# Optimization experiments

Hardware: AMD Instinct MI355X
Metric: run time of the kernel (lower is better)

## Reference

```python
import jax, jax.numpy as jnp
import numpy as np

B, P, T = 128, 196, 20
VOCAB, ENC, EMB, DEC, ATTN = 10000, 2048, 512, 512, 512


def _linear_params(key, out_dim, in_dim):
    kw, kb = jax.random.split(key)
    s = 1.0 / np.sqrt(in_dim)
    W = jax.random.uniform(kw, (out_dim, in_dim), minval=-s, maxval=s, dtype=jnp.float32)
    b = jax.random.uniform(kb, (out_dim,), minval=-s, maxval=s, dtype=jnp.float32)
    return W, b


def setup_inputs() -> dict:
    key = jax.random.key(0)
    ks = jax.random.split(key, 12)
    enc_w, enc_b = _linear_params(ks[0], ATTN, ENC)
    dec_w, dec_b = _linear_params(ks[1], ATTN, DEC)
    full_w, full_b = _linear_params(ks[2], 1, ATTN)
    W_ih, b_ih = _linear_params(ks[3], 4 * DEC, EMB + ENC)
    W_hh, b_hh = _linear_params(ks[4], 4 * DEC, DEC)
    ih_w, ih_b = _linear_params(ks[5], DEC, ENC)
    ic_w, ic_b = _linear_params(ks[6], DEC, ENC)
    fc_w, fc_b = _linear_params(ks[7], VOCAB, DEC)
    return {
        "encoder_out": jax.random.normal(ks[8], (B, P, ENC), dtype=jnp.float32),
        "captions": jax.random.randint(ks[9], (B, T), 0, VOCAB, dtype=jnp.int32),
        "lengths": jax.random.randint(ks[10], (B,), 1, T + 1, dtype=jnp.int32),
        "embedding": jax.random.normal(ks[11], (VOCAB, EMB), dtype=jnp.float32),
        "enc_attn_w": enc_w, "enc_attn_b": enc_b,
        "dec_attn_w": dec_w, "dec_attn_b": dec_b,
        "full_attn_w": full_w, "full_attn_b": full_b,
        "W_ih": W_ih, "b_ih": b_ih, "W_hh": W_hh, "b_hh": b_hh,
        "init_h_w": ih_w, "init_h_b": ih_b,
        "init_c_w": ic_w, "init_c_b": ic_b,
        "fc_w": fc_w, "fc_b": fc_b,
    }


def reference(encoder_out, captions, lengths, embedding,
              enc_attn_w, enc_attn_b, dec_attn_w, dec_attn_b,
              full_attn_w, full_attn_b, W_ih, b_ih, W_hh, b_hh,
              init_h_w, init_h_b, init_c_w, init_c_b, fc_w, fc_b):
    # init hidden state from mean-pooled encoder features
    mean_enc = encoder_out.mean(axis=1)                      # [B, ENC]
    h = mean_enc @ init_h_w.T + init_h_b                      # [B, DEC]
    c = mean_enc @ init_c_w.T + init_c_b

    # loop-invariant encoder projection for additive attention
    attn_enc = jnp.einsum('bpe,ae->bpa', encoder_out, enc_attn_w) + enc_attn_b  # [B, P, ATTN]

    embs = embedding[captions]                                # [B, T, EMB]
    embs_t = jnp.swapaxes(embs, 0, 1)                         # [T, B, EMB]

    dec = h.shape[1]

    def step(carry, emb_t):
        h, c = carry
        # additive attention
        attn_dec = h @ dec_attn_w.T + dec_attn_b              # [B, ATTN]
        energy = jnp.einsum('bpa,a->bp', jax.nn.relu(attn_enc + attn_dec[:, None, :]), full_attn_w[0]) + full_attn_b[0]
        alpha = jax.nn.softmax(energy, axis=1)                # [B, P]
        context = jnp.einsum('bpe,bp->be', encoder_out, alpha)  # [B, ENC]
        # LSTMCell
        x = jnp.concatenate([emb_t, context], axis=1)
        gates = x @ W_ih.T + b_ih + h @ W_hh.T + b_hh          # [B, 4*DEC]
        i, f, g, o = jnp.split(gates, 4, axis=1)
        c_new = jax.nn.sigmoid(f) * c + jax.nn.sigmoid(i) * jnp.tanh(g)
        h_new = jax.nn.sigmoid(o) * jnp.tanh(c_new)
        preds = h_new @ fc_w.T + fc_b                          # [B, VOCAB] (dropout in eval mode = identity)
        return (h_new, c_new), (preds, alpha)

    (_, _), (outputs_t, alphas_t) = jax.lax.scan(step, (h, c), embs_t)
    outputs = jnp.swapaxes(outputs_t, 0, 1)                   # [B, T, VOCAB]
    alphas = jnp.swapaxes(alphas_t, 0, 1)                     # [B, T, P]
    return outputs, alphas
```

## Files before the change

kernel.cpp:

```cpp
#include <hip/hip_runtime.h>

constexpr int kB = 128, kP = 196, kT = 20;
constexpr int kVocab = 10000, kEnc = 2048, kEmb = 512, kDec = 512, kAttn = 512;

typedef __bf16 b16x8 __attribute__((ext_vector_type(8)));
typedef __bf16 b16x4 __attribute__((ext_vector_type(4)));
typedef float f32x4 __attribute__((ext_vector_type(4)));
typedef unsigned short u16x4 __attribute__((ext_vector_type(4)));

__device__ __forceinline__ unsigned short f2bf(float f) {
  unsigned int u = __float_as_uint(f);
  u += 0x7fffu + ((u >> 16) & 1u);
  return (unsigned short)(u >> 16);
}
__device__ __forceinline__ float bf2f(unsigned short h) {
  return __uint_as_float(((unsigned int)h) << 16);
}

__device__ __forceinline__ void async16(const void* g, void* l) {
  __builtin_amdgcn_global_load_lds(
      (const __attribute__((address_space(1))) unsigned int*)g,
      (__attribute__((address_space(3))) unsigned int*)l, 16, 0, 0);
}

template <int MODE>
__global__ __launch_bounds__(256) void gemm128(
    const unsigned short* __restrict__ A, const unsigned short* __restrict__ W,
    const float* __restrict__ bias, unsigned short* __restrict__ Cb,
    float* __restrict__ Cf, int K, int Nv) {
  __shared__ unsigned short sA[128 * 32];
  __shared__ unsigned short sB[128 * 32];
  const int tid = threadIdx.x;
  const int lane = tid & 63, wave = tid >> 6;
  const int wm = wave >> 1, wn = wave & 1;
  const int q = lane >> 4, l = lane & 15;
  const int m0 = blockIdx.y * 128, n0 = blockIdx.x * 128;
  const int row0 = tid & 127, ch0 = tid >> 7;
  const long arow = (long)(m0 + row0) * K + ch0 * 8;
  const long brow = (long)(n0 + row0) * K + ch0 * 8;
  unsigned short* sAd0 = &sA[(ch0 * 128 + row0) * 8];
  unsigned short* sAd1 = &sA[((ch0 + 2) * 128 + row0) * 8];
  unsigned short* sBd0 = &sB[(ch0 * 128 + row0) * 8];
  unsigned short* sBd1 = &sB[((ch0 + 2) * 128 + row0) * 8];
  f32x4 acc[4][4] = {};

  for (int k0 = 0; k0 < K; k0 += 32) {
    async16(A + arow + k0, sAd0);
    async16(A + arow + k0 + 16, sAd1);
    async16(W + brow + k0, sBd0);
    async16(W + brow + k0 + 16, sBd1);
    __syncthreads();
    b16x8 af[4], bf[4];
#pragma unroll
    for (int i = 0; i < 4; i++)
      af[i] = *(const b16x8*)&sA[(q * 128 + wm * 64 + 16 * i + l) * 8];
#pragma unroll
    for (int j = 0; j < 4; j++)
      bf[j] = *(const b16x8*)&sB[(q * 128 + wn * 64 + 16 * j + l) * 8];
#pragma unroll
    for (int i = 0; i < 4; i++)
#pragma unroll
      for (int j = 0; j < 4; j++)
        acc[i][j] = __builtin_amdgcn_mfma_f32_16x16x32_bf16(af[i], bf[j], acc[i][j], 0, 0, 0);
    __syncthreads();
  }

#pragma unroll
  for (int i = 0; i < 4; i++) {
    const int row = m0 + wm * 64 + 16 * i + q * 4;
#pragma unroll
    for (int j = 0; j < 4; j++) {
      const int col = n0 + wn * 64 + 16 * j + l;
      if (col >= Nv) continue;
      const float bv = bias[col];
#pragma unroll
      for (int r = 0; r < 4; r++) {
        const float v = acc[i][j][r] + bv;
        if (MODE == 0) {
          Cb[(long)(row + r) * kAttn + col] = f2bf(v);
        } else {
          const int rr = row + r;
          Cf[((long)(rr & 127) * kT + (rr >> 7)) * (long)kVocab + col] = v;
        }
      }
    }
  }
}

template <bool A_BF16, bool OUT_BF16>
__global__ __launch_bounds__(256) void gemm_bt(
    const void* __restrict__ A_, const unsigned short* __restrict__ W,
    const float* __restrict__ bias, float* __restrict__ C,
    unsigned short* __restrict__ Cb, int M, int N, int K, long ldc) {
  const int lane = threadIdx.x & 63;
  const int wave = threadIdx.x >> 6;
  const int wm = wave >> 1, wn = wave & 1;
  const int m0 = blockIdx.y * 64 + wm * 32;
  const int n0 = blockIdx.x * 64 + wn * 32;
  const int q = lane >> 4;
  const int l = lane & 15;
  f32x4 acc[2][2] = {};
  const unsigned short* Ab = (const unsigned short*)A_;
  const float* Af = (const float*)A_;

  for (int k0 = 0; k0 < K; k0 += 32) {
    const int ka = k0 + q * 8;
    b16x8 af[2], wf[2];
#pragma unroll
    for (int i = 0; i < 2; i++) {
      int r = m0 + 16 * i + l;
      if (r >= M) r = M - 1;
      if (A_BF16) {
        af[i] = *(const b16x8*)(Ab + (long)r * K + ka);
      } else {
        const float* p = Af + (long)r * K + ka;
        const f32x4 lo = *(const f32x4*)p;
        const f32x4 hi = *(const f32x4*)(p + 4);
        b16x8 t;
#pragma unroll
        for (int j = 0; j < 4; j++) {
          ((unsigned short*)&t)[j] = f2bf(lo[j]);
          ((unsigned short*)&t)[4 + j] = f2bf(hi[j]);
        }
        af[i] = t;
      }
    }
#pragma unroll
    for (int j = 0; j < 2; j++) {
      int r = n0 + 16 * j + l;
      if (r >= N) r = N - 1;
      wf[j] = *(const b16x8*)(W + (long)r * K + ka);
    }
#pragma unroll
    for (int i = 0; i < 2; i++)
#pragma unroll
      for (int j = 0; j < 2; j++)
        acc[i][j] = __builtin_amdgcn_mfma_f32_16x16x32_bf16(af[i], wf[j], acc[i][j], 0, 0, 0);
  }

#pragma unroll
  for (int i = 0; i < 2; i++)
#pragma unroll
    for (int j = 0; j < 2; j++) {
      const int col = n0 + 16 * j + l;
      if (col >= N) continue;
      const float bv = bias ? bias[col] : 0.0f;
#pragma unroll
      for (int r = 0; r < 4; r++) {
        const int row = m0 + 16 * i + q * 4 + r;
        if (row >= M) continue;
        const float v = acc[i][j][r] + bv;
        if (OUT_BF16) Cb[(long)row * ldc + col] = f2bf(v);
        else          C[(long)row * ldc + col] = v;
      }
    }
}

__global__ __launch_bounds__(256) void adfc_kernel(
    const unsigned short* __restrict__ h_bf,
    const unsigned short* __restrict__ daw, const float* __restrict__ dab,
    float* __restrict__ ad_out,
    const unsigned short* __restrict__ fcw, const float* __restrict__ fcb,
    float* __restrict__ preds, long pred_ld) {
  const int blk = blockIdx.x;
  const unsigned short* W;
  const float* bias;
  float* out;
  long ldc;
  int N, m0, n0;
  if (blk < 16) {
    if (!ad_out) return;
    W = daw; bias = dab; out = ad_out; ldc = 512; N = 512;
    n0 = (blk & 7) * 64; m0 = (blk >> 3) * 64;
  } else {
    if (!preds) return;
    const int idx = blk - 16;
    W = fcw; bias = fcb; out = preds; ldc = pred_ld; N = kVocab;
    n0 = (idx % 157) * 64; m0 = (idx / 157) * 64;
  }
  const int lane = threadIdx.x & 63, wave = threadIdx.x >> 6;
  const int wm = wave >> 1, wn = wave & 1;
  const int q = lane >> 4, l = lane & 15;
  const int mi = m0 + wm * 32, ni = n0 + wn * 32;
  f32x4 acc[2][2] = {};

  for (int k0 = 0; k0 < 512; k0 += 64) {
    b16x8 af[2][2], wf[2][2];
#pragma unroll
    for (int u = 0; u < 2; u++) {
      const int ka = k0 + u * 32 + q * 8;
#pragma unroll
      for (int i = 0; i < 2; i++)
        af[u][i] = *(const b16x8*)(h_bf + (long)(mi + 16 * i + l) * 512 + ka);
#pragma unroll
      for (int j = 0; j < 2; j++) {
        int r = ni + 16 * j + l;
        if (r >= N) r = N - 1;
        wf[u][j] = *(const b16x8*)(W + (long)r * 512 + ka);
      }
    }
#pragma unroll
    for (int u = 0; u < 2; u++)
#pragma unroll
      for (int i = 0; i < 2; i++)
#pragma unroll
        for (int j = 0; j < 2; j++)
          acc[i][j] = __builtin_amdgcn_mfma_f32_16x16x32_bf16(af[u][i], wf[u][j], acc[i][j], 0, 0, 0);
  }
#pragma unroll
  for (int i = 0; i < 2; i++)
#pragma unroll
    for (int j = 0; j < 2; j++) {
      const int col = ni + 16 * j + l;
      if (col >= N) continue;
      const float bv = bias[col];
#pragma unroll
      for (int r = 0; r < 4; r++) {
        const int row = mi + 16 * i + q * 4 + r;
        out[(long)row * ldc + col] = acc[i][j][r] + bv;
      }
    }
}

template <bool SRC_BF16>
__global__ __launch_bounds__(256) void attn2(
    const void* __restrict__ enc_, const unsigned short* __restrict__ attn_enc_bf,
    const float* __restrict__ ad_g, const float* __restrict__ faw,
    const float* __restrict__ fab, float* __restrict__ alphas,
    unsigned short* __restrict__ ctx, int t) {
  const int b = blockIdx.x;
  const int half = blockIdx.y;
  const int tid = threadIdx.x;
  const int lane = tid & 63, wave = tid >> 6;
  __shared__ float ad_s[512];
  __shared__ float e_sm[kP];
  __shared__ float red[4];
  __shared__ float cred[128][8];

  ad_s[tid] = ad_g[b * kAttn + tid];
  ad_s[tid + 256] = ad_g[b * kAttn + tid + 256];
  __syncthreads();

  float ad8[8], w8[8];
  const int a0 = lane * 8;
#pragma unroll
  for (int j = 0; j < 8; j++) { ad8[j] = ad_s[a0 + j]; w8[j] = faw[a0 + j]; }
  const float fb0 = fab[0];
  for (int p = wave; p < kP; p += 4) {
    const b16x8 rv = *(const b16x8*)(attn_enc_bf + ((long)(b * kP + p)) * kAttn + a0);
    float s = 0.f;
#pragma unroll
    for (int j = 0; j < 8; j++)
      s += w8[j] * fmaxf(bf2f(((const unsigned short*)&rv)[j]) + ad8[j], 0.f);
#pragma unroll
    for (int off = 32; off > 0; off >>= 1) s += __shfl_down(s, off, 64);
    if (lane == 0) e_sm[p] = s + fb0;
  }
  __syncthreads();

  const float v = (tid < kP) ? e_sm[tid] : -3.0e38f;
  float m = v;
#pragma unroll
  for (int off = 32; off > 0; off >>= 1) m = fmaxf(m, __shfl_down(m, off, 64));
  if (lane == 0) red[wave] = m;
  __syncthreads();
  m = fmaxf(fmaxf(red[0], red[1]), fmaxf(red[2], red[3]));
  const float ex = (tid < kP) ? expf(v - m) : 0.f;
  float s = ex;
#pragma unroll
  for (int off = 32; off > 0; off >>= 1) s += __shfl_down(s, off, 64);
  if (lane == 0) red[wave] = s;
  __syncthreads();
  s = red[0] + red[1] + red[2] + red[3];
  __syncthreads();
  const float alpha = ex / s;
  if (tid < kP) {
    e_sm[tid] = alpha;
    if (half == 0) alphas[((long)b * kT + t) * kP + tid] = alpha;
  }
  __syncthreads();

  const int pg = tid >> 7, th = tid & 127;
  const int e = half * 1024 + th * 8;
  float a8[8] = {};
  if (SRC_BF16) {
    const unsigned short* base = (const unsigned short*)enc_ + (long)b * kP * kEnc + e;
    const int pbeg = pg * 98;
#pragma unroll 2
    for (int p = pbeg; p < pbeg + 98; p++) {
      const float a = e_sm[p];
      const b16x8 rv = *(const b16x8*)(base + (long)p * kEnc);
#pragma unroll
      for (int j = 0; j < 8; j++) a8[j] += a * bf2f(((const unsigned short*)&rv)[j]);
    }
  } else {
    const float* base = (const float*)enc_ + (long)b * kP * kEnc + e;
    const int pbeg = pg * 98;
#pragma unroll 2
    for (int p = pbeg; p < pbeg + 98; p++) {
      const float a = e_sm[p];
      const f32x4 lo = *(const f32x4*)(base + (long)p * kEnc);
      const f32x4 hi = *(const f32x4*)(base + (long)p * kEnc + 4);
#pragma unroll
      for (int j = 0; j < 4; j++) { a8[j] += a * lo[j]; a8[4 + j] += a * hi[j]; }
    }
  }
  if (pg == 1) {
#pragma unroll
    for (int j = 0; j < 8; j++) cred[th][j] = a8[j];
  }
  __syncthreads();
  if (pg == 0) {
    u16x4 o0, o1;
#pragma unroll
    for (int j = 0; j < 4; j++) {
      o0[j] = f2bf(a8[j] + cred[th][j]);
      o1[j] = f2bf(a8[4 + j] + cred[th][4 + j]);
    }
    *(u16x4*)(ctx + (long)b * kEnc + e) = o0;
    *(u16x4*)(ctx + (long)b * kEnc + e + 4) = o1;
  }
}

__global__ __launch_bounds__(256) void gemm_gates(
    const unsigned short* __restrict__ embs_t, const unsigned short* __restrict__ ctx,
    const unsigned short* __restrict__ hbf, const unsigned short* __restrict__ Wih,
    const unsigned short* __restrict__ Whh, float* __restrict__ gates_part) {
  const int lane = threadIdx.x & 63;
  const int wave = threadIdx.x >> 6;
  const int wm = wave >> 1, wn = wave & 1;
  const int m0 = blockIdx.y * 64 + wm * 32;
  const int n0 = blockIdx.x * 64 + wn * 32;
  const int z = blockIdx.z;
  const int q = lane >> 4;
  const int l = lane & 15;
  f32x4 acc[2][2] = {};
  float* gout = gates_part + (long)z * kB * 2048;

  const int kbeg = z * 768, kend = kbeg + 768;
  for (int k0 = kbeg; k0 < kend; k0 += 32) {
    b16x8 af[2], wf[2];
#pragma unroll
    for (int i = 0; i < 2; i++) {
      const int r = m0 + 16 * i + l;
      const unsigned short* p;
      if (k0 < 512)        p = embs_t + (long)r * kEmb + k0;
      else if (k0 < 2560)  p = ctx + (long)r * kEnc + (k0 - 512);
      else                 p = hbf + (long)r * kDec + (k0 - 2560);
      af[i] = *(const b16x8*)(p + q * 8);
    }
#pragma unroll
    for (int j = 0; j < 2; j++) {
      const int r = n0 + 16 * j + l;
      const unsigned short* p;
      if (k0 < 2560) p = Wih + (long)r * 2560 + k0;
      else           p = Whh + (long)r * 512 + (k0 - 2560);
      wf[j] = *(const b16x8*)(p + q * 8);
    }
#pragma unroll
    for (int i = 0; i < 2; i++)
#pragma unroll
      for (int j = 0; j < 2; j++)
        acc[i][j] = __builtin_amdgcn_mfma_f32_16x16x32_bf16(af[i], wf[j], acc[i][j], 0, 0, 0);
  }
#pragma unroll
  for (int i = 0; i < 2; i++)
#pragma unroll
    for (int j = 0; j < 2; j++) {
      const int col = n0 + 16 * j + l;
#pragma unroll
      for (int r = 0; r < 4; r++) {
        const int row = m0 + 16 * i + q * 4 + r;
        gout[(long)row * 2048 + col] = acc[i][j][r];
      }
    }
}

__global__ __launch_bounds__(256) void lstm_pw(
    const float* __restrict__ gp, const float* __restrict__ bsum,
    float* __restrict__ c, float* __restrict__ h, unsigned short* __restrict__ hbf) {
  const int idx = blockIdx.x * 256 + threadIdx.x;
  const int b = idx >> 9, d = idx & 511;
  float g4[4];
#pragma unroll
  for (int g = 0; g < 4; g++) {
    const int col = g * 512 + d;
    float s = bsum[col];
#pragma unroll
    for (int z = 0; z < 4; z++) s += gp[(long)z * kB * 2048 + (long)b * 2048 + col];
    g4[g] = s;
  }
  const float si = 1.f / (1.f + expf(-g4[0]));
  const float sf = 1.f / (1.f + expf(-g4[1]));
  const float so = 1.f / (1.f + expf(-g4[3]));
  const float cn = sf * c[idx] + si * tanhf(g4[2]);
  const float hn = so * tanhf(cn);
  c[idx] = cn;
  h[idx] = hn;
  hbf[idx] = f2bf(hn);
}

template <bool SRC_BF16>
__global__ __launch_bounds__(256) void mean_kernel(
    const void* __restrict__ enc_, unsigned short* __restrict__ mean_bf) {
  const int b = blockIdx.x;
  const int e = threadIdx.x * 8;
  float acc[8] = {};
  if (SRC_BF16) {
    const unsigned short* base = (const unsigned short*)enc_ + (long)b * kP * kEnc + e;
    for (int p = 0; p < kP; p++) {
      const b16x8 v = *(const b16x8*)(base + (long)p * kEnc);
#pragma unroll
      for (int j = 0; j < 8; j++) acc[j] += bf2f(((const unsigned short*)&v)[j]);
    }
  } else {
    const float* base = (const float*)enc_ + (long)b * kP * kEnc + e;
    for (int p = 0; p < kP; p++) {
      const f32x4 lo = *(const f32x4*)(base + (long)p * kEnc);
      const f32x4 hi = *(const f32x4*)(base + (long)p * kEnc + 4);
#pragma unroll
      for (int j = 0; j < 4; j++) { acc[j] += lo[j]; acc[4 + j] += hi[j]; }
    }
  }
#pragma unroll
  for (int j = 0; j < 8; j++)
    mean_bf[(long)b * kEnc + e + j] = f2bf(acc[j] * (1.0f / 196.0f));
}

__global__ __launch_bounds__(256) void f32_to_bf16_vec(
    const float* __restrict__ src, unsigned short* __restrict__ dst, long n4) {
  for (long i = blockIdx.x * (long)blockDim.x + threadIdx.x; i < n4;
       i += (long)gridDim.x * blockDim.x) {
    const f32x4 v = *(const f32x4*)(src + i * 4);
    u16x4 o;
#pragma unroll
    for (int j = 0; j < 4; j++) o[j] = f2bf(v[j]);
    *(u16x4*)(dst + i * 4) = o;
  }
}

__global__ __launch_bounds__(256) void gather_emb(
    const float* __restrict__ embedding, const int* __restrict__ captions,
    unsigned short* __restrict__ embs) {
  const int r = blockIdx.x;
  const int t = r >> 7, b = r & 127;
  const int cap = captions[b * kT + t];
  const float* src = embedding + (long)cap * kEmb;
  unsigned short* dst = embs + (long)r * kEmb;
  for (int i = threadIdx.x; i < kEmb; i += 256) dst[i] = f2bf(src[i]);
}

__global__ void bias_sum_k(const float* __restrict__ b1, const float* __restrict__ b2,
                           float* __restrict__ o) {
  const int i = blockIdx.x * 256 + threadIdx.x;
  if (i < 2048) o[i] = b1[i] + b2[i];
}

extern "C" void kernel_launch(void* const* d_in, const int* in_sizes, int n_in,
                              void* d_out, int out_size, void* d_ws, size_t ws_size,
                              hipStream_t stream) {
  const float* enc = (const float*)d_in[0];
  const int* captions = (const int*)d_in[1];
  const float* embedding = (const float*)d_in[3];
  const float* eaw = (const float*)d_in[4];
  const float* eab = (const float*)d_in[5];
  const float* daw = (const float*)d_in[6];
  const float* dab = (const float*)d_in[7];
  const float* faw = (const float*)d_in[8];
  const float* fab = (const float*)d_in[9];
  const float* Wih = (const float*)d_in[10];
  const float* bih = (const float*)d_in[11];
  const float* Whh = (const float*)d_in[12];
  const float* bhh = (const float*)d_in[13];
  const float* ihw = (const float*)d_in[14];
  const float* ihb = (const float*)d_in[15];
  const float* icw = (const float*)d_in[16];
  const float* icb = (const float*)d_in[17];
  const float* fcw = (const float*)d_in[18];
  const float* fcb = (const float*)d_in[19];

  float* out = (float*)d_out;
  float* alphas = out + (long)kB * kT * kVocab;

  char* ws = (char*)d_ws;
  size_t off = 0;
  auto alloc = [&](size_t bytes) -> void* {
    void* p = ws + off;
    off = (off + bytes + 255) & ~(size_t)255;
    return p;
  };
  unsigned short* attn_enc_bf = (unsigned short*)alloc((size_t)kB * kP * kAttn * 2);
  unsigned short* Wih_bf = (unsigned short*)alloc((size_t)2048 * 2560 * 2);
  unsigned short* Whh_bf = (unsigned short*)alloc((size_t)2048 * 512 * 2);
  unsigned short* fcw_bf = (unsigned short*)alloc((size_t)kVocab * kDec * 2);
  unsigned short* eaw_bf = (unsigned short*)alloc((size_t)kAttn * kEnc * 2);
  unsigned short* daw_bf = (unsigned short*)alloc((size_t)kAttn * kDec * 2);
  unsigned short* ihw_bf = (unsigned short*)alloc((size_t)kDec * kEnc * 2);
  unsigned short* icw_bf = (unsigned short*)alloc((size_t)kDec * kEnc * 2);
  unsigned short* embs_bf = (unsigned short*)alloc((size_t)kT * kB * kEmb * 2);
  unsigned short* mean_bf = (unsigned short*)alloc((size_t)kB * kEnc * 2);
  float* h = (float*)alloc((size_t)kB * kDec * 4);
  float* c = (float*)alloc((size_t)kB * kDec * 4);
  unsigned short* h_hist = (unsigned short*)alloc((size_t)(kT + 1) * kB * kDec * 2);
  float* ad_buf = (float*)alloc((size_t)kB * kAttn * 4);
  unsigned short* ctx_bf = (unsigned short*)alloc((size_t)kB * kEnc * 2);
  float* gates_part = (float*)alloc((size_t)4 * kB * 2048 * 4);
  float* bsum = (float*)alloc((size_t)2048 * 4);
  unsigned short* enc_bf = (unsigned short*)alloc((size_t)kB * kP * kEnc * 2);
  const bool have_enc_bf = (off <= ws_size);

  auto cvt = [&](const float* s, unsigned short* d, long n) {
    const long n4 = n / 4;
    long g = (n4 + 255) / 256;
    if (g > 2048) g = 2048;
    f32_to_bf16_vec<<<dim3((unsigned)g), dim3(256), 0, stream>>>(s, d, n4);
  };

  cvt(eaw, eaw_bf, (long)kAttn * kEnc);
  cvt(daw, daw_bf, (long)kAttn * kDec);
  cvt(Wih, Wih_bf, (long)2048 * 2560);
  cvt(Whh, Whh_bf, (long)2048 * 512);
  cvt(fcw, fcw_bf, (long)kVocab * kDec);
  cvt(ihw, ihw_bf, (long)kDec * kEnc);
  cvt(icw, icw_bf, (long)kDec * kEnc);
  if (have_enc_bf) cvt(enc, enc_bf, (long)kB * kP * kEnc);
  bias_sum_k<<<8, 256, 0, stream>>>(bih, bhh, bsum);
  gather_emb<<<kT * kB, 256, 0, stream>>>(embedding, captions, embs_bf);
  if (have_enc_bf)
    mean_kernel<true><<<kB, 256, 0, stream>>>(enc_bf, mean_bf);
  else
    mean_kernel<false><<<kB, 256, 0, stream>>>(enc, mean_bf);

  gemm_bt<true, false><<<dim3(kDec / 64, kB / 64), 256, 0, stream>>>(
      mean_bf, ihw_bf, ihb, h, (unsigned short*)nullptr, kB, kDec, kEnc, kDec);
  gemm_bt<true, false><<<dim3(kDec / 64, kB / 64), 256, 0, stream>>>(
      mean_bf, icw_bf, icb, c, (unsigned short*)nullptr, kB, kDec, kEnc, kDec);
  cvt(h, h_hist, (long)kB * kDec);

  if (have_enc_bf)
    gemm128<0><<<dim3(kAttn / 128, (kB * kP) / 128), 256, 0, stream>>>(
        enc_bf, eaw_bf, eab, attn_enc_bf, (float*)nullptr, kEnc, kAttn);
  else
    gemm_bt<false, true><<<dim3(kAttn / 64, (kB * kP) / 64), 256, 0, stream>>>(
        enc, eaw_bf, eab, (float*)nullptr, attn_enc_bf, kB * kP, kAttn, kEnc, kAttn);

  for (int t = 0; t < kT; t++) {
    const unsigned short* hcur = h_hist + (long)t * kB * kDec;

    adfc_kernel<<<16, 256, 0, stream>>>(
        hcur, daw_bf, dab, ad_buf, fcw_bf, fcb, (float*)nullptr, 0);

    if (have_enc_bf)
      attn2<true><<<dim3(kB, 2), 256, 0, stream>>>(
          enc_bf, attn_enc_bf, ad_buf, faw, fab, alphas, ctx_bf, t);
    else
      attn2<false><<<dim3(kB, 2), 256, 0, stream>>>(
          enc, attn_enc_bf, ad_buf, faw, fab, alphas, ctx_bf, t);

    gemm_gates<<<dim3(2048 / 64, kB / 64, 4), 256, 0, stream>>>(
        embs_bf + (long)t * kB * kEmb, ctx_bf, hcur, Wih_bf, Whh_bf, gates_part);

    lstm_pw<<<(kB * kDec) / 256, 256, 0, stream>>>(
        gates_part, bsum, c, h, h_hist + (long)(t + 1) * kB * kDec);
  }

  gemm128<1><<<dim3((kVocab + 127) / 128, kT * kB / 128), 256, 0, stream>>>(
      h_hist + (long)kB * kDec, fcw_bf, fcb, (unsigned short*)nullptr, out, kDec, kVocab);
}
```

Before: 2.200 ms.

## Fuse decoder attention projection into LSTM pointwise kernel, double-buffer gemm128 loads

Removes the per-step adfc launch by having the LSTM pointwise kernel (now one block per batch row) compute the next step's decoder attention projection from the new hidden state with a scalar dot-product loop. The initial projection is computed once before the loop. The gemm128 kernel gets double-buffered LDS staging so the next K-tile loads while the current one is multiplied, plus an XCD-aware workgroup remapping. The fused projection uses scalar FMAs rather than MFMA and no longer writes the fp32 h array, so per-block work in the pointwise kernel grows.

```diff
diff --git a/kernel.cpp b/kernel.cpp
--- a/kernel.cpp
+++ b/kernel.cpp
@@ -28,41 +28,52 @@
     const unsigned short* __restrict__ A, const unsigned short* __restrict__ W,
     const float* __restrict__ bias, unsigned short* __restrict__ Cb,
     float* __restrict__ Cf, int K, int Nv) {
-  __shared__ unsigned short sA[128 * 32];
-  __shared__ unsigned short sB[128 * 32];
+  __shared__ unsigned short sA[2][128 * 32];
+  __shared__ unsigned short sB[2][128 * 32];
   const int tid = threadIdx.x;
   const int lane = tid & 63, wave = tid >> 6;
   const int wm = wave >> 1, wn = wave & 1;
   const int q = lane >> 4, l = lane & 15;
-  const int m0 = blockIdx.y * 128, n0 = blockIdx.x * 128;
+  const int nwg = gridDim.x * gridDim.y;
+  const int orig = blockIdx.y * gridDim.x + blockIdx.x;
+  const int qc = nwg >> 3, rc = nwg & 7;
+  const int xcd = orig & 7, o8 = orig >> 3;
+  const int wg = (xcd < rc ? xcd * (qc + 1) : rc * (qc + 1) + (xcd - rc) * qc) + o8;
+  const int m0 = (wg / gridDim.x) * 128, n0 = (wg % gridDim.x) * 128;
   const int row0 = tid & 127, ch0 = tid >> 7;
   const long arow = (long)(m0 + row0) * K + ch0 * 8;
   const long brow = (long)(n0 + row0) * K + ch0 * 8;
-  unsigned short* sAd0 = &sA[(ch0 * 128 + row0) * 8];
-  unsigned short* sAd1 = &sA[((ch0 + 2) * 128 + row0) * 8];
-  unsigned short* sBd0 = &sB[(ch0 * 128 + row0) * 8];
-  unsigned short* sBd1 = &sB[((ch0 + 2) * 128 + row0) * 8];
   f32x4 acc[4][4] = {};
 
+  auto stage = [&](int buf, int k0) {
+    async16(A + arow + k0, &sA[buf][(ch0 * 128 + row0) * 8]);
+    async16(A + arow + k0 + 16, &sA[buf][((ch0 + 2) * 128 + row0) * 8]);
+    async16(W + brow + k0, &sB[buf][(ch0 * 128 + row0) * 8]);
+    async16(W + brow + k0 + 16, &sB[buf][((ch0 + 2) * 128 + row0) * 8]);
+  };
+
+  stage(0, 0);
+  __syncthreads();
+  int cur = 0;
   for (int k0 = 0; k0 < K; k0 += 32) {
-    async16(A + arow + k0, sAd0);
-    async16(A + arow + k0 + 16, sAd1);
-    async16(W + brow + k0, sBd0);
-    async16(W + brow + k0 + 16, sBd1);
-    __syncthreads();
-    b16x8 af[4], bf[4];
+    const bool last = (k0 + 32 >= K);
+    if (!last) stage(cur ^ 1, k0 + 32);
+    b16x8 af[4], bfr[4];
 #pragma unroll
     for (int i = 0; i < 4; i++)
-      af[i] = *(const b16x8*)&sA[(q * 128 + wm * 64 + 16 * i + l) * 8];
+      af[i] = *(const b16x8*)&sA[cur][(q * 128 + wm * 64 + 16 * i + l) * 8];
 #pragma unroll
     for (int j = 0; j < 4; j++)
-      bf[j] = *(const b16x8*)&sB[(q * 128 + wn * 64 + 16 * j + l) * 8];
+      bfr[j] = *(const b16x8*)&sB[cur][(q * 128 + wn * 64 + 16 * j + l) * 8];
 #pragma unroll
     for (int i = 0; i < 4; i++)
 #pragma unroll
       for (int j = 0; j < 4; j++)
-        acc[i][j] = __builtin_amdgcn_mfma_f32_16x16x32_bf16(af[i], bf[j], acc[i][j], 0, 0, 0);
-    __syncthreads();
+        acc[i][j] = __builtin_amdgcn_mfma_f32_16x16x32_bf16(af[i], bfr[j], acc[i][j], 0, 0, 0);
+    if (!last) {
+      __syncthreads();
+      cur ^= 1;
+    }
   }
 
 #pragma unroll
@@ -159,25 +170,9 @@
 __global__ __launch_bounds__(256) void adfc_kernel(
     const unsigned short* __restrict__ h_bf,
     const unsigned short* __restrict__ daw, const float* __restrict__ dab,
-    float* __restrict__ ad_out,
-    const unsigned short* __restrict__ fcw, const float* __restrict__ fcb,
-    float* __restrict__ preds, long pred_ld) {
+    float* __restrict__ ad_out) {
   const int blk = blockIdx.x;
-  const unsigned short* W;
-  const float* bias;
-  float* out;
-  long ldc;
-  int N, m0, n0;
-  if (blk < 16) {
-    if (!ad_out) return;
-    W = daw; bias = dab; out = ad_out; ldc = 512; N = 512;
-    n0 = (blk & 7) * 64; m0 = (blk >> 3) * 64;
-  } else {
-    if (!preds) return;
-    const int idx = blk - 16;
-    W = fcw; bias = fcb; out = preds; ldc = pred_ld; N = kVocab;
-    n0 = (idx % 157) * 64; m0 = (idx / 157) * 64;
-  }
+  const int n0 = (blk & 7) * 64, m0 = (blk >> 3) * 64;
   const int lane = threadIdx.x & 63, wave = threadIdx.x >> 6;
   const int wm = wave >> 1, wn = wave & 1;
   const int q = lane >> 4, l = lane & 15;
@@ -193,11 +188,8 @@
       for (int i = 0; i < 2; i++)
         af[u][i] = *(const b16x8*)(h_bf + (long)(mi + 16 * i + l) * 512 + ka);
 #pragma unroll
-      for (int j = 0; j < 2; j++) {
-        int r = ni + 16 * j + l;
-        if (r >= N) r = N - 1;
-        wf[u][j] = *(const b16x8*)(W + (long)r * 512 + ka);
-      }
+      for (int j = 0; j < 2; j++)
+        wf[u][j] = *(const b16x8*)(daw + (long)(ni + 16 * j + l) * 512 + ka);
     }
 #pragma unroll
     for (int u = 0; u < 2; u++)
@@ -212,12 +204,11 @@
 #pragma unroll
     for (int j = 0; j < 2; j++) {
       const int col = ni + 16 * j + l;
-      if (col >= N) continue;
-      const float bv = bias[col];
+      const float bv = dab[col];
 #pragma unroll
       for (int r = 0; r < 4; r++) {
         const int row = mi + 16 * i + q * 4 + r;
-        out[(long)row * ldc + col] = acc[i][j][r] + bv;
+        ad_out[(long)row * 512 + col] = acc[i][j][r] + bv;
       }
     }
 }
@@ -376,28 +367,54 @@
     }
 }
 
-__global__ __launch_bounds__(256) void lstm_pw(
+__global__ __launch_bounds__(256) void lstm_ad(
     const float* __restrict__ gp, const float* __restrict__ bsum,
-    float* __restrict__ c, float* __restrict__ h, unsigned short* __restrict__ hbf) {
-  const int idx = blockIdx.x * 256 + threadIdx.x;
-  const int b = idx >> 9, d = idx & 511;
-  float g4[4];
-#pragma unroll
-  for (int g = 0; g < 4; g++) {
-    const int col = g * 512 + d;
-    float s = bsum[col];
-#pragma unroll
-    for (int z = 0; z < 4; z++) s += gp[(long)z * kB * 2048 + (long)b * 2048 + col];
-    g4[g] = s;
-  }
-  const float si = 1.f / (1.f + expf(-g4[0]));
-  const float sf = 1.f / (1.f + expf(-g4[1]));
-  const float so = 1.f / (1.f + expf(-g4[3]));
-  const float cn = sf * c[idx] + si * tanhf(g4[2]);
-  const float hn = so * tanhf(cn);
-  c[idx] = cn;
-  h[idx] = hn;
-  hbf[idx] = f2bf(hn);
+    float* __restrict__ c, unsigned short* __restrict__ h_out,
+    const unsigned short* __restrict__ daw, const float* __restrict__ dab,
+    float* __restrict__ ad_out) {
+  const int b = blockIdx.x;
+  const int tid = threadIdx.x;
+  __shared__ unsigned short h_s[512];
+
+#pragma unroll
+  for (int u = 0; u < 2; u++) {
+    const int d = tid + u * 256;
+    float g4[4];
+#pragma unroll
+    for (int g = 0; g < 4; g++) {
+      const int col = g * 512 + d;
+      float s = bsum[col];
+#pragma unroll
+      for (int z = 0; z < 4; z++) s += gp[(long)z * kB * 2048 + (long)b * 2048 + col];
+      g4[g] = s;
+    }
+    const float si = 1.f / (1.f + expf(-g4[0]));
+    const float sf = 1.f / (1.f + expf(-g4[1]));
+    const float so = 1.f / (1.f + expf(-g4[3]));
+    const long idx = (long)b * 512 + d;
+    const float cn = sf * c[idx] + si * tanhf(g4[2]);
+    const float hn = so * tanhf(cn);
+    c[idx] = cn;
+    const unsigned short hb = f2bf(hn);
+    h_out[idx] = hb;
+    h_s[d] = hb;
+  }
+  __syncthreads();
+
+#pragma unroll
+  for (int u = 0; u < 2; u++) {
+    const int r = tid + u * 256;
+    const unsigned short* wr = daw + (long)r * 512;
+    float s = 0.f;
+    for (int k = 0; k < 512; k += 8) {
+      const b16x8 hv = *(const b16x8*)&h_s[k];
+      const b16x8 wv = *(const b16x8*)(wr + k);
+#pragma unroll
+      for (int j = 0; j < 8; j++)
+        s += bf2f(((const unsigned short*)&hv)[j]) * bf2f(((const unsigned short*)&wv)[j]);
+    }
+    ad_out[(long)b * 512 + r] = s + dab[r];
+  }
 }
 
 template <bool SRC_BF16>
@@ -544,11 +561,10 @@
     gemm_bt<false, true><<<dim3(kAttn / 64, (kB * kP) / 64), 256, 0, stream>>>(
         enc, eaw_bf, eab, (float*)nullptr, attn_enc_bf, kB * kP, kAttn, kEnc, kAttn);
 
+  adfc_kernel<<<16, 256, 0, stream>>>(h_hist, daw_bf, dab, ad_buf);
+
   for (int t = 0; t < kT; t++) {
     const unsigned short* hcur = h_hist + (long)t * kB * kDec;
-
-    adfc_kernel<<<16, 256, 0, stream>>>(
-        hcur, daw_bf, dab, ad_buf, fcw_bf, fcb, (float*)nullptr, 0);
 
     if (have_enc_bf)
       attn2<true><<<dim3(kB, 2), 256, 0, stream>>>(
@@ -560,8 +576,8 @@
     gemm_gates<<<dim3(2048 / 64, kB / 64, 4), 256, 0, stream>>>(
         embs_bf + (long)t * kB * kEmb, ctx_bf, hcur, Wih_bf, Whh_bf, gates_part);
 
-    lstm_pw<<<(kB * kDec) / 256, 256, 0, stream>>>(
-        gates_part, bsum, c, h, h_hist + (long)(t + 1) * kB * kDec);
+    lstm_ad<<<kB, 256, 0, stream>>>(
+        gates_part, bsum, c, h_hist + (long)(t + 1) * kB * kDec, daw_bf, dab, ad_buf);
   }
 
   gemm128<1><<<dim3((kVocab + 127) / 128, kT * kB / 128), 256, 0, stream>>>(
```

Measured after the change: 2.366 ms. 7.6% more time.
